# Performance work log

Hardware: AMD Instinct MI355X
Metric: run time of the kernel (lower is better)

## Reference

```python
import jax, jax.numpy as jnp
import numpy as np

B, C, D, W, H = 4, 256, 32, 32, 32  # img_dim = D, in_channels = C, model_num = 4


def setup_inputs() -> dict:
    key = jax.random.key(0)
    ks = jax.random.split(key, 8)
    s = 0.02
    inp = {
        "m1": jax.random.normal(ks[0], (B, C, D, W, H), jnp.float32),
        "m2": jax.random.normal(ks[1], (B, C, D, W, H), jnp.float32),
        "m3": jax.random.normal(ks[2], (B, C, D, W, H), jnp.float32),
        "m4": jax.random.normal(ks[3], (B, C, D, W, H), jnp.float32),
        # nn.Linear weights (torch convention: y = x @ W.T + b)
        "Wq": jax.random.normal(ks[4], (D, D), jnp.float32) * s,
        "bq": jnp.zeros((D,), jnp.float32),
        "Wk": jax.random.normal(ks[5], (D, D), jnp.float32) * s,
        "bk": jnp.zeros((D,), jnp.float32),
        # four 1x1x1 Conv3d kernels, squeezed to [model, out_c, in_c]
        "Wc": jax.random.normal(ks[6], (4, C, C), jnp.float32) * s,
        "bc": jnp.zeros((4, C), jnp.float32),
    }
    return inp


def reference(m1, m2, m3, m4, Wq, bq, Wk, bk, Wc, bc):
    d = m1.shape[2]
    # adaptive_avg_pool3d(x, (D,1,1)) == mean over W,H -> [B,C,D]; stack 4 modalities -> [B,C,4,D]
    pooled = jnp.stack([m.mean(axis=(3, 4)) for m in (m1, m2, m3, m4)], axis=2)
    q = jnp.einsum('bcd,ed->bce', pooled[:, :, 0], Wq) + bq          # [B,C,D]
    k = jnp.einsum('bcmd,ed->bcme', pooled, Wk) + bk                 # [B,C,4,D]
    # per-modality attention logits: q . k_m over D -> [B,C,4]
    a = jnp.einsum('bcd,bcmd->bcm', q, k) / jnp.sqrt(jnp.float32(d))
    a = jax.nn.softmax(a, axis=-1)                                   # [B,C,4]
    ms = jnp.stack([m1, m2, m3, m4], axis=0)                         # [4,B,C,D,W,H]
    # 1x1x1 Conv3d == channel-mixing GEMM per voxel
    conv = jnp.einsum('mbcdwh,moc->mbodwh', ms, Wc) + bc[:, None, :, None, None, None]
    # weighted sum of the 4 conv outputs by per-(B,C) attention weights
    out = jnp.einsum('bcm,mbcdwh->bcdwh', a, conv)                   # [B,C,D,W,H]
    return out
```

## Files before the change

### kernel.cpp

```cpp
#include <hip/hip_runtime.h>
#include <hip/hip_bf16.h>

#define NB 4
#define NC 256
#define ND 32
#define WH 1024
#define DWH 32768
#define KTOT 1024

typedef __attribute__((ext_vector_type(8))) short short8;
typedef __attribute__((ext_vector_type(4))) float f32x4;

static __device__ __forceinline__ unsigned short f32_to_bf16(float f) {
    unsigned u = __builtin_bit_cast(unsigned, f);
    u = u + 0x7fff + ((u >> 16) & 1);
    return (unsigned short)(u >> 16);
}

static __device__ __forceinline__ unsigned pack_bf16x2(float lo, float hi) {
    __hip_bfloat162 h = __float22bfloat162_rn(make_float2(lo, hi));
    unsigned u;
    __builtin_memcpy(&u, &h, 4);
    return u;
}

__global__ __launch_bounds__(256) void pool_kernel(
    const float* __restrict__ i0, const float* __restrict__ i1,
    const float* __restrict__ i2, const float* __restrict__ i3,
    float* __restrict__ pooled)
{
    int bid = blockIdx.x;
    int m   = bid & 3;
    int bc  = bid >> 2;
    const float* src = (m == 0 ? i0 : m == 1 ? i1 : m == 2 ? i2 : i3)
                       + (size_t)bc * DWH;
    int t = threadIdx.x;
    int d   = t >> 3;
    int sub = t & 7;

    const float4* row = (const float4*)(src + (size_t)d * WH);
    float4 a0 = {0.f, 0.f, 0.f, 0.f}, a1 = {0.f, 0.f, 0.f, 0.f};
    #pragma unroll
    for (int j = 0; j < 16; ++j) {
        float4 u = row[sub + 8 * (2 * j)];
        float4 w = row[sub + 8 * (2 * j + 1)];
        a0.x += u.x; a0.y += u.y; a0.z += u.z; a0.w += u.w;
        a1.x += w.x; a1.y += w.y; a1.z += w.z; a1.w += w.w;
    }
    float s = (a0.x + a0.y) + (a0.z + a0.w) + (a1.x + a1.y) + (a1.z + a1.w);
    s += __shfl_down(s, 4, 64);
    s += __shfl_down(s, 2, 64);
    s += __shfl_down(s, 1, 64);
    if (sub == 0) pooled[bc * 128 + m * 32 + d] = s * (1.0f / 1024.0f);
}

__global__ __launch_bounds__(64) void attn_kernel(
    const float* __restrict__ pooled,
    const float* __restrict__ Wq, const float* __restrict__ bq,
    const float* __restrict__ Wk, const float* __restrict__ bk,
    const float* __restrict__ Wc, const float* __restrict__ bcv,
    unsigned short* __restrict__ Amat, float* __restrict__ beff)
{
    int bc_idx = blockIdx.x;
    int lane = threadIdx.x;
    int e = lane & 31;
    const float* P = pooled + bc_idx * 128;

    float q = 0.f, kv[4] = {0.f, 0.f, 0.f, 0.f};
    for (int d = 0; d < 32; ++d) {
        float pq = P[d];
        float wq = Wq[e * 32 + d], wk = Wk[e * 32 + d];
        q += pq * wq;
        #pragma unroll
        for (int m = 0; m < 4; ++m) kv[m] += P[m * 32 + d] * wk;
    }
    q += bq[e];
    #pragma unroll
    for (int m = 0; m < 4; ++m) kv[m] += bk[e];

    float lg[4];
    #pragma unroll
    for (int m = 0; m < 4; ++m) {
        float p = q * kv[m];
        #pragma unroll
        for (int off = 16; off; off >>= 1) p += __shfl_xor(p, off, 32);
        lg[m] = p * 0.17677669529663687f;
    }
    float mx = fmaxf(fmaxf(lg[0], lg[1]), fmaxf(lg[2], lg[3]));
    float ex[4], s = 0.f;
    #pragma unroll
    for (int m = 0; m < 4; ++m) { ex[m] = __expf(lg[m] - mx); s += ex[m]; }
    float a[4];
    #pragma unroll
    for (int m = 0; m < 4; ++m) a[m] = ex[m] / s;

    int c = bc_idx & 255;
    if (lane == 0) {
        float be = 0.f;
        #pragma unroll
        for (int m = 0; m < 4; ++m) be += a[m] * bcv[m * NC + c];
        beff[bc_idx] = be;
    }
    unsigned short* Arow = Amat + (size_t)bc_idx * KTOT;
    #pragma unroll
    for (int j = 0; j < 16; ++j) {
        int k = j * 64 + lane;
        int m = k >> 8, cin = k & 255;
        float v = a[m] * Wc[(m * NC + c) * NC + cin];
        Arow[k] = f32_to_bf16(v);
    }
}

#define BM 128
#define BN 128
#define BK 64

static __device__ __forceinline__ int swzA(int row, int chunk) {
    return row * 64 + ((chunk ^ (row & 7)) << 3);
}
static __device__ __forceinline__ int swzB(int row, int chunk) {
    return row * 64 + ((chunk ^ ((row >> 1) & 7)) << 3);
}

__global__ __launch_bounds__(256, 3) void gemm_kernel(
    const float* __restrict__ i0, const float* __restrict__ i1,
    const float* __restrict__ i2, const float* __restrict__ i3,
    const unsigned short* __restrict__ Amat,
    const float* __restrict__ beff,
    float* __restrict__ out)
{
    __shared__ __align__(16) short As[2 * BM * BK];
    __shared__ __align__(16) short Bs[BN * BK];

    int raw = blockIdx.x;
    int sb  = (raw & 7) * 256 + (raw >> 3);
    int ot = sb & 1;
    int xt = (sb >> 1) & 255;
    int b  = sb >> 9;
    int o0 = ot * BM, x0 = xt * BN;

    const unsigned short* Ab = Amat + ((size_t)b * NC + o0) * KTOT;

    int t = threadIdx.x;
    int wave = t >> 6, lane = t & 63;
    int wr = wave >> 1, wc = wave & 1;
    int lrow = lane & 15, lk = lane >> 4;

    f32x4 acc[4][4];
    #pragma unroll
    for (int mi = 0; mi < 4; ++mi)
        #pragma unroll
        for (int ni = 0; ni < 4; ++ni)
            acc[mi][ni] = (f32x4){0.f, 0.f, 0.f, 0.f};

    int xq = t & 31;
    int kb = (t >> 5) * 8;

    int ar = wave * 32 + (lane >> 3);
    int aq = (lane & 7) ^ (lane >> 3);
    const unsigned short* asrc = Ab + (size_t)ar * KTOT + aq * 8;

    float4 v[8];

    {
        #pragma unroll
        for (int p = 0; p < 4; ++p)
            __builtin_amdgcn_global_load_lds(
                (const __attribute__((address_space(1))) unsigned int*)
                    (asrc + (size_t)p * 8 * KTOT),
                (__attribute__((address_space(3))) unsigned int*)
                    (As + (wave * 32 + p * 8) * 64),
                16, 0, 0);
        const float* Bb = i0 + (size_t)b * NC * DWH + x0;
        #pragma unroll
        for (int j = 0; j < 8; ++j)
            v[j] = *(const float4*)(Bb + (size_t)(kb + j) * DWH + xq * 4);
    }

    #pragma unroll 1
    for (int it = 0; it < KTOT / BK; ++it) {
        const short* Acur = As + (it & 1) * (BM * BK);
        short* Anx = As + ((it + 1) & 1) * (BM * BK);

        __builtin_amdgcn_s_barrier();
        __builtin_amdgcn_sched_barrier(0);

        {
            int ja = (it + 1 < 16) ? it + 1 : 15;
            #pragma unroll
            for (int p = 0; p < 4; ++p)
                __builtin_amdgcn_global_load_lds(
                    (const __attribute__((address_space(1))) unsigned int*)
                        (asrc + (size_t)p * 8 * KTOT + ja * BK),
                    (__attribute__((address_space(3))) unsigned int*)
                        (Anx + (wave * 32 + p * 8) * 64),
                    16, 0, 0);
        }
        __builtin_amdgcn_sched_barrier(0);

        uint4 pk[4];
        #pragma unroll
        for (int i = 0; i < 4; ++i) {
            unsigned w[4];
            #pragma unroll
            for (int j = 0; j < 4; ++j)
                w[j] = pack_bf16x2(((const float*)&v[2 * j])[i],
                                   ((const float*)&v[2 * j + 1])[i]);
            pk[i] = (uint4){w[0], w[1], w[2], w[3]};
        }

        {
            int itn = (it < 15) ? it + 1 : 15;
            int m = itn >> 2, cbase = (itn & 3) * 64;
            const float* Bb = (m == 0 ? i0 : m == 1 ? i1 : m == 2 ? i2 : i3)
                              + ((size_t)b * NC + cbase) * DWH + x0;
            #pragma unroll
            for (int j = 0; j < 8; ++j)
                v[j] = *(const float4*)(Bb + (size_t)(kb + j) * DWH + xq * 4);
        }
        __builtin_amdgcn_sched_barrier(0);

        #pragma unroll
        for (int i = 0; i < 4; ++i)
            *(uint4*)(&Bs[swzB(xq * 4 + i, t >> 5)]) = pk[i];

        asm volatile("s_waitcnt vmcnt(12) lgkmcnt(0)" ::: "memory");
        __builtin_amdgcn_s_barrier();
        __builtin_amdgcn_sched_barrier(0);

        #pragma unroll
        for (int kk = 0; kk < 2; ++kk) {
            int q = kk * 4 + lk;
            short8 af[4], bf[4];
            #pragma unroll
            for (int mi = 0; mi < 4; ++mi) {
                int r = wr * 64 + mi * 16 + lrow;
                af[mi] = *(const short8*)(&Acur[swzA(r, q)]);
            }
            #pragma unroll
            for (int ni = 0; ni < 4; ++ni) {
                int x = wc * 64 + ni * 16 + lrow;
                bf[ni] = *(const short8*)(&Bs[swzB(x, q)]);
            }
            __builtin_amdgcn_s_setprio(1);
            #pragma unroll
            for (int mi = 0; mi < 4; ++mi)
                #pragma unroll
                for (int ni = 0; ni < 4; ++ni)
                    acc[mi][ni] = __builtin_amdgcn_mfma_f32_16x16x32_bf16(
                        af[mi], bf[ni], acc[mi][ni], 0, 0, 0);
            __builtin_amdgcn_s_setprio(0);
        }
    }

    const float* beff_b = beff + b * NC + o0;
    float* outb = out + ((size_t)b * NC + o0) * DWH + x0;
    #pragma unroll
    for (int mi = 0; mi < 4; ++mi) {
        #pragma unroll
        for (int r4 = 0; r4 < 4; ++r4) {
            int row = wr * 64 + mi * 16 + lk * 4 + r4;
            float bias = beff_b[row];
            float* orow = outb + (size_t)row * DWH;
            #pragma unroll
            for (int ni = 0; ni < 4; ++ni) {
                int col = wc * 64 + ni * 16 + lrow;
                orow[col] = acc[mi][ni][r4] + bias;
            }
        }
    }
}

extern "C" void kernel_launch(void* const* d_in, const int* in_sizes, int n_in,
                              void* d_out, int out_size, void* d_ws, size_t ws_size,
                              hipStream_t stream) {
    const float* m1 = (const float*)d_in[0];
    const float* m2 = (const float*)d_in[1];
    const float* m3 = (const float*)d_in[2];
    const float* m4 = (const float*)d_in[3];
    const float* Wq = (const float*)d_in[4];
    const float* bq = (const float*)d_in[5];
    const float* Wk = (const float*)d_in[6];
    const float* bk = (const float*)d_in[7];
    const float* Wc = (const float*)d_in[8];
    const float* bcv = (const float*)d_in[9];
    float* out = (float*)d_out;

    float* pooled        = (float*)d_ws;
    unsigned short* Amat = (unsigned short*)((char*)d_ws + 524288);
    float* beff          = (float*)((char*)d_ws + 524288 + 2097152);

    pool_kernel<<<NB * NC * 4, 256, 0, stream>>>(m1, m2, m3, m4, pooled);
    attn_kernel<<<NB * NC, 64, 0, stream>>>(pooled, Wq, bq, Wk, bk, Wc, bcv,
                                            Amat, beff);
    gemm_kernel<<<(NB) * (NC / BM) * (DWH / BN), 256, 0, stream>>>(
        m1, m2, m3, m4, Amat, beff, out);
}
```

Before: 249.1 us.

## Fuse pooling with bf16 transpose of inputs and feed GEMM via async LDS loads

Adds a transpool kernel that reads the four input modalities once. It computes the pooled means and also writes a bf16, K-major tiled copy of the activations into workspace. A new GEMM kernel then streams both A and B tiles with global_load_lds double buffering, so the per-iteration fp32 load, bf16 pack and LDS store of B are gone. This costs an extra 256MB bf16 write plus a read-back, and it runs only when the workspace is large enough; otherwise the old path is used.

```diff
diff --git a/kernel.cpp b/kernel.cpp
--- a/kernel.cpp
+++ b/kernel.cpp
@@ -22,6 +22,90 @@
     unsigned u;
     __builtin_memcpy(&u, &h, 4);
     return u;
+}
+
+__global__ __launch_bounds__(256) void transpool_kernel(
+    const float* __restrict__ i0, const float* __restrict__ i1,
+    const float* __restrict__ i2, const float* __restrict__ i3,
+    unsigned short* __restrict__ Bt, float* __restrict__ pooled)
+{
+    __shared__ float lds[64 * 132];
+    int bid = blockIdx.x;
+    int d  = bid & 31;
+    int cb = (bid >> 5) & 3;
+    int m  = (bid >> 7) & 3;
+    int b  = bid >> 9;
+    const float* base = (m == 0 ? i0 : m == 1 ? i1 : m == 2 ? i2 : i3)
+                        + ((size_t)(b * NC + cb * 64)) * DWH + d * WH;
+    int t  = threadIdx.x;
+    int rl = t >> 3;
+    int xo = t & 7;
+    int xr = t >> 1;
+    int ch = t & 1;
+
+    float pc0 = 0.f, pc1 = 0.f;
+    float4 v0[4], v1[4];
+
+    #pragma unroll
+    for (int j = 0; j < 4; ++j) {
+        v0[j] = *(const float4*)(base + (size_t)rl * DWH + (xo + 8 * j) * 4);
+        v1[j] = *(const float4*)(base + (size_t)(32 + rl) * DWH + (xo + 8 * j) * 4);
+    }
+    #pragma unroll
+    for (int j = 0; j < 4; ++j) {
+        pc0 += v0[j].x + v0[j].y + v0[j].z + v0[j].w;
+        pc1 += v1[j].x + v1[j].y + v1[j].z + v1[j].w;
+        *(float4*)&lds[rl * 132 + (xo + 8 * j) * 4]        = v0[j];
+        *(float4*)&lds[(32 + rl) * 132 + (xo + 8 * j) * 4] = v1[j];
+    }
+    __syncthreads();
+
+    unsigned short* tb0 = Bt + (((size_t)b * 256 + d * 8) * 16 + (m * 4 + cb)) * 8192;
+
+    #pragma unroll 1
+    for (int s = 0; s < 8; ++s) {
+        if (s < 7) {
+            const float* bs = base + (s + 1) * 128;
+            #pragma unroll
+            for (int j = 0; j < 4; ++j) {
+                v0[j] = *(const float4*)(bs + (size_t)rl * DWH + (xo + 8 * j) * 4);
+                v1[j] = *(const float4*)(bs + (size_t)(32 + rl) * DWH + (xo + 8 * j) * 4);
+            }
+        }
+        {
+            unsigned short* dst = tb0 + (size_t)s * 16 * 8192 + (size_t)xr * 64 + ch * 32;
+            unsigned pk[16];
+            #pragma unroll
+            for (int i = 0; i < 16; ++i) {
+                float f0 = lds[(ch * 32 + 2 * i) * 132 + xr];
+                float f1 = lds[(ch * 32 + 2 * i + 1) * 132 + xr];
+                pk[i] = pack_bf16x2(f0, f1);
+            }
+            #pragma unroll
+            for (int u = 0; u < 4; ++u)
+                *(uint4*)(dst + u * 8) =
+                    (uint4){pk[4 * u], pk[4 * u + 1], pk[4 * u + 2], pk[4 * u + 3]};
+        }
+        __syncthreads();
+        if (s < 7) {
+            #pragma unroll
+            for (int j = 0; j < 4; ++j) {
+                pc0 += v0[j].x + v0[j].y + v0[j].z + v0[j].w;
+                pc1 += v1[j].x + v1[j].y + v1[j].z + v1[j].w;
+                *(float4*)&lds[rl * 132 + (xo + 8 * j) * 4]        = v0[j];
+                *(float4*)&lds[(32 + rl) * 132 + (xo + 8 * j) * 4] = v1[j];
+            }
+            __syncthreads();
+        }
+    }
+
+    pc0 += __shfl_down(pc0, 4, 64); pc1 += __shfl_down(pc1, 4, 64);
+    pc0 += __shfl_down(pc0, 2, 64); pc1 += __shfl_down(pc1, 2, 64);
+    pc0 += __shfl_down(pc0, 1, 64); pc1 += __shfl_down(pc1, 1, 64);
+    if (xo == 0) {
+        pooled[((size_t)b * NC + cb * 64 + rl) * 128 + m * 32 + d]      = pc0 * (1.0f / 1024.0f);
+        pooled[((size_t)b * NC + cb * 64 + 32 + rl) * 128 + m * 32 + d] = pc1 * (1.0f / 1024.0f);
+    }
 }
 
 __global__ __launch_bounds__(256) void pool_kernel(
@@ -122,6 +206,124 @@
     return row * 64 + ((chunk ^ ((row >> 1) & 7)) << 3);
 }
 
+__global__ __launch_bounds__(256, 2) void gemm2_kernel(
+    const unsigned short* __restrict__ Amat,
+    const unsigned short* __restrict__ Bt,
+    const float* __restrict__ beff,
+    float* __restrict__ out)
+{
+    __shared__ __align__(16) short As[2 * BM * BK];
+    __shared__ __align__(16) short Bs[2 * BN * BK];
+
+    int raw = blockIdx.x;
+    int sb  = (raw & 7) * 256 + (raw >> 3);
+    int ot = sb & 1;
+    int xt = (sb >> 1) & 255;
+    int b  = sb >> 9;
+    int o0 = ot * BM, x0 = xt * BN;
+
+    int t = threadIdx.x;
+    int wave = t >> 6, lane = t & 63;
+    int wr = wave >> 1, wc = wave & 1;
+    int lrow = lane & 15, lk = lane >> 4;
+    int lr8 = lane >> 3;
+    int aq  = (lane & 7) ^ lr8;
+
+    const unsigned short* asrc = Amat + ((size_t)b * NC + o0) * KTOT
+                                 + (size_t)(wave * 32 + lr8) * KTOT + aq * 8;
+    const unsigned short* bsrc = Bt + ((size_t)b * 256 + xt) * 16 * 8192
+                                 + (size_t)(wave * 32 + lr8) * 64 + aq * 8;
+
+    f32x4 acc[4][4];
+    #pragma unroll
+    for (int mi = 0; mi < 4; ++mi)
+        #pragma unroll
+        for (int ni = 0; ni < 4; ++ni)
+            acc[mi][ni] = (f32x4){0.f, 0.f, 0.f, 0.f};
+
+    #pragma unroll
+    for (int p = 0; p < 4; ++p)
+        __builtin_amdgcn_global_load_lds(
+            (const __attribute__((address_space(1))) unsigned int*)
+                (asrc + (size_t)p * 8 * KTOT),
+            (__attribute__((address_space(3))) unsigned int*)
+                (As + (wave * 32 + p * 8) * 64), 16, 0, 0);
+    #pragma unroll
+    for (int p = 0; p < 4; ++p)
+        __builtin_amdgcn_global_load_lds(
+            (const __attribute__((address_space(1))) unsigned int*)
+                (bsrc + (size_t)p * 8 * 64),
+            (__attribute__((address_space(3))) unsigned int*)
+                (Bs + (wave * 32 + p * 8) * 64), 16, 0, 0);
+    __builtin_amdgcn_sched_barrier(0);
+
+    #pragma unroll 1
+    for (int it = 0; it < 16; ++it) {
+        int ja = (it < 15) ? it + 1 : 15;
+        int bo = ((it + 1) & 1) * (BM * BK);
+        #pragma unroll
+        for (int p = 0; p < 4; ++p)
+            __builtin_amdgcn_global_load_lds(
+                (const __attribute__((address_space(1))) unsigned int*)
+                    (asrc + (size_t)p * 8 * KTOT + ja * BK),
+                (__attribute__((address_space(3))) unsigned int*)
+                    (As + bo + (wave * 32 + p * 8) * 64), 16, 0, 0);
+        #pragma unroll
+        for (int p = 0; p < 4; ++p)
+            __builtin_amdgcn_global_load_lds(
+                (const __attribute__((address_space(1))) unsigned int*)
+                    (bsrc + (size_t)ja * 8192 + p * 8 * 64),
+                (__attribute__((address_space(3))) unsigned int*)
+                    (Bs + bo + (wave * 32 + p * 8) * 64), 16, 0, 0);
+        __builtin_amdgcn_sched_barrier(0);
+
+        asm volatile("s_waitcnt vmcnt(8)" ::: "memory");
+        __builtin_amdgcn_s_barrier();
+        __builtin_amdgcn_sched_barrier(0);
+
+        const short* Acur = As + (it & 1) * (BM * BK);
+        const short* Bcur = Bs + (it & 1) * (BM * BK);
+        #pragma unroll
+        for (int kk = 0; kk < 2; ++kk) {
+            int q = kk * 4 + lk;
+            short8 af[4], bf[4];
+            #pragma unroll
+            for (int mi = 0; mi < 4; ++mi)
+                af[mi] = *(const short8*)(&Acur[swzA(wr * 64 + mi * 16 + lrow, q)]);
+            #pragma unroll
+            for (int ni = 0; ni < 4; ++ni)
+                bf[ni] = *(const short8*)(&Bcur[swzA(wc * 64 + ni * 16 + lrow, q)]);
+            __builtin_amdgcn_s_setprio(1);
+            #pragma unroll
+            for (int mi = 0; mi < 4; ++mi)
+                #pragma unroll
+                for (int ni = 0; ni < 4; ++ni)
+                    acc[mi][ni] = __builtin_amdgcn_mfma_f32_16x16x32_bf16(
+                        af[mi], bf[ni], acc[mi][ni], 0, 0, 0);
+            __builtin_amdgcn_s_setprio(0);
+        }
+        __builtin_amdgcn_s_barrier();
+        __builtin_amdgcn_sched_barrier(0);
+    }
+
+    const float* beff_b = beff + b * NC + o0;
+    float* outb = out + ((size_t)b * NC + o0) * DWH + x0;
+    #pragma unroll
+    for (int mi = 0; mi < 4; ++mi) {
+        #pragma unroll
+        for (int r4 = 0; r4 < 4; ++r4) {
+            int row = wr * 64 + mi * 16 + lk * 4 + r4;
+            float bias = beff_b[row];
+            float* orow = outb + (size_t)row * DWH;
+            #pragma unroll
+            for (int ni = 0; ni < 4; ++ni) {
+                int col = wc * 64 + ni * 16 + lrow;
+                orow[col] = acc[mi][ni][r4] + bias;
+            }
+        }
+    }
+}
+
 __global__ __launch_bounds__(256, 3) void gemm_kernel(
     const float* __restrict__ i0, const float* __restrict__ i1,
     const float* __restrict__ i2, const float* __restrict__ i3,
@@ -169,8 +371,7 @@
                 (const __attribute__((address_space(1))) unsigned int*)
                     (asrc + (size_t)p * 8 * KTOT),
                 (__attribute__((address_space(3))) unsigned int*)
-                    (As + (wave * 32 + p * 8) * 64),
-                16, 0, 0);
+                    (As + (wave * 32 + p * 8) * 64), 16, 0, 0);
         const float* Bb = i0 + (size_t)b * NC * DWH + x0;
         #pragma unroll
         for (int j = 0; j < 8; ++j)
@@ -193,8 +394,7 @@
                     (const __attribute__((address_space(1))) unsigned int*)
                         (asrc + (size_t)p * 8 * KTOT + ja * BK),
                     (__attribute__((address_space(3))) unsigned int*)
-                        (Anx + (wave * 32 + p * 8) * 64),
-                    16, 0, 0);
+                        (Anx + (wave * 32 + p * 8) * 64), 16, 0, 0);
         }
         __builtin_amdgcn_sched_barrier(0);
 
@@ -233,15 +433,11 @@
             int q = kk * 4 + lk;
             short8 af[4], bf[4];
             #pragma unroll
-            for (int mi = 0; mi < 4; ++mi) {
-                int r = wr * 64 + mi * 16 + lrow;
-                af[mi] = *(const short8*)(&Acur[swzA(r, q)]);
-            }
-            #pragma unroll
-            for (int ni = 0; ni < 4; ++ni) {
-                int x = wc * 64 + ni * 16 + lrow;
-                bf[ni] = *(const short8*)(&Bs[swzB(x, q)]);
-            }
+            for (int mi = 0; mi < 4; ++mi)
+                af[mi] = *(const short8*)(&Acur[swzA(wr * 64 + mi * 16 + lrow, q)]);
+            #pragma unroll
+            for (int ni = 0; ni < 4; ++ni)
+                bf[ni] = *(const short8*)(&Bs[swzB(wc * 64 + ni * 16 + lrow, q)]);
             __builtin_amdgcn_s_setprio(1);
             #pragma unroll
             for (int mi = 0; mi < 4; ++mi)
@@ -286,13 +482,28 @@
     const float* bcv = (const float*)d_in[9];
     float* out = (float*)d_out;
 
-    float* pooled        = (float*)d_ws;
-    unsigned short* Amat = (unsigned short*)((char*)d_ws + 524288);
-    float* beff          = (float*)((char*)d_ws + 524288 + 2097152);
-
-    pool_kernel<<<NB * NC * 4, 256, 0, stream>>>(m1, m2, m3, m4, pooled);
-    attn_kernel<<<NB * NC, 64, 0, stream>>>(pooled, Wq, bq, Wk, bk, Wc, bcv,
-                                            Amat, beff);
-    gemm_kernel<<<(NB) * (NC / BM) * (DWH / BN), 256, 0, stream>>>(
-        m1, m2, m3, m4, Amat, beff, out);
-}
+    const size_t BT_BYTES = (size_t)NB * KTOT * DWH * 2;
+    const size_t NEED = BT_BYTES + 524288 + 2097152 + 4096;
+
+    if (ws_size >= NEED) {
+        unsigned short* Btr   = (unsigned short*)d_ws;
+        float* pooled         = (float*)((char*)d_ws + BT_BYTES);
+        unsigned short* Amat  = (unsigned short*)((char*)d_ws + BT_BYTES + 524288);
+        float* beff           = (float*)((char*)d_ws + BT_BYTES + 524288 + 2097152);
+
+        transpool_kernel<<<2048, 256, 0, stream>>>(m1, m2, m3, m4, Btr, pooled);
+        attn_kernel<<<NB * NC, 64, 0, stream>>>(pooled, Wq, bq, Wk, bk, Wc, bcv,
+                                                Amat, beff);
+        gemm2_kernel<<<2048, 256, 0, stream>>>(Amat, Btr, beff, out);
+    } else {
+        float* pooled        = (float*)d_ws;
+        unsigned short* Amat = (unsigned short*)((char*)d_ws + 524288);
+        float* beff          = (float*)((char*)d_ws + 524288 + 2097152);
+
+        pool_kernel<<<NB * NC * 4, 256, 0, stream>>>(m1, m2, m3, m4, pooled);
+        attn_kernel<<<NB * NC, 64, 0, stream>>>(pooled, Wq, bq, Wk, bk, Wc, bcv,
+                                                Amat, beff);
+        gemm_kernel<<<(NB) * (NC / BM) * (DWH / BN), 256, 0, stream>>>(
+            m1, m2, m3, m4, Amat, beff, out);
+    }
+}
```

After: 305.9 us. 1.23x slower.
